# Optimization experiments

Hardware: AMD Instinct MI355X
Metric: run time of the kernel (lower is better)

Reference implementation:

```python
import jax, jax.numpy as jnp
import numpy as np

N = 50000
E = 800000
IN_C, HID, OUT_C = 128, 128, 40
EPS = 1e-5  # BatchNorm eps


def setup_inputs() -> dict:
    key = jax.random.key(0)
    ks = jax.random.split(key, 8)
    x = jax.random.normal(ks[0], (N, IN_C), dtype=jnp.float32)
    edge_index = jax.random.randint(ks[1], (2, E), 0, N, dtype=jnp.int64)
    s1 = 1.0 / np.sqrt(IN_C)
    s2 = 1.0 / np.sqrt(HID)
    return {
        "x": x,
        "edge_index": edge_index,
        "W1": jax.random.uniform(ks[2], (IN_C, HID), jnp.float32, -s1, s1),
        "b1": jnp.zeros((HID,), jnp.float32),
        "g1": jnp.ones((HID,), jnp.float32),
        "beta1": jnp.zeros((HID,), jnp.float32),
        "W2": jax.random.uniform(ks[3], (HID, HID), jnp.float32, -s2, s2),
        "b2": jnp.zeros((HID,), jnp.float32),
        "g2": jnp.ones((HID,), jnp.float32),
        "beta2": jnp.zeros((HID,), jnp.float32),
        "W3": jax.random.uniform(ks[4], (HID, OUT_C), jnp.float32, -s2, s2),
        "b3": jnp.zeros((OUT_C,), jnp.float32),
    }


def _gcn_norm(src, dst, num_nodes):
    # symmetric normalization D^-1/2 A D^-1/2, no self loops, unit edge weights
    deg = jax.ops.segment_sum(jnp.ones_like(dst, dtype=jnp.float32), dst,
                              num_segments=num_nodes)
    dinv = jnp.where(deg > 0, jax.lax.rsqrt(jnp.maximum(deg, 1.0)), 0.0)
    return dinv[src] * dinv[dst]  # [E]


def _conv(h, W, b, src, dst, norm, num_nodes):
    h = h @ W  # linear transform first (fewer message features)
    msg = norm[:, None] * h[src]  # [E, F] gather
    out = jax.ops.segment_sum(msg, dst, num_segments=num_nodes)  # scatter-add
    return out + b


def _bn_relu(h, g, beta):
    mu = jnp.mean(h, axis=0)
    var = jnp.mean(jnp.square(h - mu), axis=0)  # biased, as torch BN
    hn = (h - mu) * jax.lax.rsqrt(var + EPS) * g + beta
    return jax.nn.relu(hn)


def reference(x, edge_index, W1, b1, g1, beta1, W2, b2, g2, beta2, W3, b3):
    src, dst = edge_index[0], edge_index[1]
    norm = _gcn_norm(src, dst, N)  # cached=True: shared across layers
    h = _bn_relu(_conv(x, W1, b1, src, dst, norm, N), g1, beta1)
    h = _bn_relu(_conv(h, W2, b2, src, dst, norm, N), g2, beta2)
    return _conv(h, W3, b3, src, dst, norm, N)
```

## Files before the change

kernel.cpp:

```cpp
#include <hip/hip_runtime.h>
#include <hip/hip_fp16.h>

typedef _Float16 half8 __attribute__((ext_vector_type(8)));
typedef float floatx4 __attribute__((ext_vector_type(4)));


__device__ __forceinline__ void unpack8(uint4 v, float* f) {
    const __half2* hp = (const __half2*)&v;
    float2 a = __half22float2(hp[0]);
    float2 b = __half22float2(hp[1]);
    float2 c = __half22float2(hp[2]);
    float2 d = __half22float2(hp[3]);
    f[0] = a.x; f[1] = a.y; f[2] = b.x; f[3] = b.y;
    f[4] = c.x; f[5] = c.y; f[6] = d.x; f[7] = d.y;
}

__device__ __forceinline__ uint4 pack8(const float* f) {
    __half2 h0 = __floats2half2_rn(f[0], f[1]);
    __half2 h1 = __floats2half2_rn(f[2], f[3]);
    __half2 h2 = __floats2half2_rn(f[4], f[5]);
    __half2 h3 = __floats2half2_rn(f[6], f[7]);
    uint4 v;
    v.x = *(const unsigned int*)&h0;
    v.y = *(const unsigned int*)&h1;
    v.z = *(const unsigned int*)&h2;
    v.w = *(const unsigned int*)&h3;
    return v;
}

__global__ void k_zeroz(int* p, int n) {
    int i = blockIdx.x * 256 + threadIdx.x;
    if (i < n) p[i] = 0;
}


__global__ void k_packW3(const float* __restrict__ W1, const float* __restrict__ W2,
                         const float* __restrict__ W3, __half* __restrict__ Wt1,
                         __half* __restrict__ Wt2, __half* __restrict__ Wt3) {
    int i = blockIdx.x * 256 + threadIdx.x;
    if (i < 128 * 128) {
        int n = i >> 7, k = i & 127;
        Wt1[i] = __float2half(W1[(size_t)k * 128 + n]);
    } else if (i < 2 * 128 * 128) {
        int j = i - 128 * 128;
        int n = j >> 7, k = j & 127;
        Wt2[j] = __float2half(W2[(size_t)k * 128 + n]);
    } else if (i < 2 * 128 * 128 + 48 * 128) {
        int j = i - 2 * 128 * 128;
        int n = j >> 7, k = j & 127;
        Wt3[j] = (n < 40) ? __float2half(W3[(size_t)k * 40 + n]) : __half(0.f);
    }
}


__global__ void k_deg_xcd(const int* __restrict__ dst, int* __restrict__ deg,
                          int E, int rs) {
    int lo = (blockIdx.x & 7) * rs;
    int i = (blockIdx.x >> 3) * 256 + threadIdx.x;
    if (i < E) {
        int d = dst[i];
        if (d >= lo && d < lo + rs) atomicAdd(&deg[d], 1);
    }
}

__global__ void k_place_xcd(const int* __restrict__ src, const int* __restrict__ dst,
                            int* __restrict__ cursor, unsigned short* __restrict__ sidx,
                            int E, int rs) {
    int lo = (blockIdx.x & 7) * rs;
    int i = (blockIdx.x >> 3) * 256 + threadIdx.x;
    if (i < E) {
        int d = dst[i];
        if (d >= lo && d < lo + rs) {
            int pos = atomicAdd(&cursor[d], 1);
            sidx[pos] = (unsigned short)src[i];
        }
    }
}

__global__ __launch_bounds__(256) void k_chunkscan(const int* __restrict__ deg,
                                                   int* __restrict__ bsum, int n) {
    __shared__ int ls[256];
    int t = threadIdx.x;
    int s = 0;
    int base = t * 256;
    for (int k = 0; k < 256; ++k) {
        int idx = base + k;
        if (idx < n) s += deg[idx];
    }
    ls[t] = s;
    __syncthreads();
    for (int off = 1; off < 256; off <<= 1) {
        int v = t >= off ? ls[t - off] : 0;
        __syncthreads();
        ls[t] += v;
        __syncthreads();
    }
    bsum[t] = ls[t] - s;
}

__global__ void k_scanchunk(const int* __restrict__ cnt, const int* __restrict__ bsum,
                            int* __restrict__ row_ptr, int* __restrict__ cursor,
                            float* __restrict__ dinv, int n, int E) {
    __shared__ int ls[256];
    int i = blockIdx.x * 256 + threadIdx.x;
    int v = i < n ? cnt[i] : 0;
    ls[threadIdx.x] = v;
    __syncthreads();
    for (int off = 1; off < 256; off <<= 1) {
        int t = threadIdx.x >= off ? ls[threadIdx.x - off] : 0;
        __syncthreads();
        ls[threadIdx.x] += t;
        __syncthreads();
    }
    if (i < n) {
        int ex = ls[threadIdx.x] - v + bsum[blockIdx.x];
        row_ptr[i] = ex;
        cursor[i] = ex;
        dinv[i] = v > 0 ? rsqrtf((float)v) : 0.f;
    }
    if (i == n - 1) row_ptr[n] = E;
}


template <int CT, int STRIDE, int VALID, int AMODE, int CSPLIT>
__global__ __launch_bounds__(256) void k_gemm_mfma(const void* __restrict__ Ap,
                                                   const __half* __restrict__ Wt,
                                                   const float* __restrict__ sums32,
                                                   const float* __restrict__ sumsq32,
                                                   const float* __restrict__ g,
                                                   const float* __restrict__ beta,
                                                   const float* __restrict__ dinv,
                                                   __half* __restrict__ C, int nrows) {
    __shared__ char lw[CT * 16 * 256];
    __shared__ float lsc[128], lsh[128];
    const int rowblk = (CSPLIT == 2) ? (blockIdx.x >> 1) : blockIdx.x;
    const int colblk = (CSPLIT == 2) ? (blockIdx.x & 1) : 0;

    const int nu4 = CT * 16 * 16;
    for (int i = threadIdx.x; i < nu4; i += 256) {
        int row = i >> 4, k8 = i & 15;
        uint4 v = ((const uint4*)Wt)[(colblk * CT * 16 + row) * 16 + k8];
        *(uint4*)(lw + ((row * 256 + k8 * 16) ^ ((row & 7) << 4))) = v;
    }
    if (AMODE == 1 && threadIdx.x < 128) {
        int c = threadIdx.x;
        float s = 0.f, q = 0.f;
        for (int k2 = 0; k2 < 32; ++k2) {
            s += sums32[k2 * 128 + c];
            q += sumsq32[k2 * 128 + c];
        }
        float inv_n = 1.f / (float)nrows;
        float mu = s * inv_n;
        float var = q * inv_n - mu * mu;
        float rs = rsqrtf(var + 1e-5f);
        float sc = rs * g[c];
        lsc[c] = sc;
        lsh[c] = beta[c] - mu * sc;
    }
    __syncthreads();

    const int lane = threadIdx.x & 63;
    const int wid = threadIdx.x >> 6;
    const int l15 = lane & 15;
    const int lg = lane >> 4;
    const int rowbase = rowblk * 128 + wid * 32;

    half8 a2[2][4];
#pragma unroll
    for (int r = 0; r < 2; ++r) {
        int row = rowbase + r * 16 + l15;
        bool ok = row < nrows;
#pragma unroll
        for (int kk = 0; kk < 4; ++kk) {
            const int c0 = kk * 32 + lg * 8;
            half8 h = {0, 0, 0, 0, 0, 0, 0, 0};
            if (ok) {
                if (AMODE == 0) {
                    const float* a = (const float*)Ap + (size_t)row * 128 + c0;
                    float4 v0 = *(const float4*)a;
                    float4 v1 = *(const float4*)(a + 4);
                    h[0] = (_Float16)v0.x; h[1] = (_Float16)v0.y;
                    h[2] = (_Float16)v0.z; h[3] = (_Float16)v0.w;
                    h[4] = (_Float16)v1.x; h[5] = (_Float16)v1.y;
                    h[6] = (_Float16)v1.z; h[7] = (_Float16)v1.w;
                } else {
                    uint4 raw = *(const uint4*)((const __half*)Ap + (size_t)row * 128 + c0);
                    float f[8];
                    unpack8(raw, f);
                    float4 s0 = *(const float4*)&lsc[c0];
                    float4 s1 = *(const float4*)&lsc[c0 + 4];
                    float4 t0 = *(const float4*)&lsh[c0];
                    float4 t1 = *(const float4*)&lsh[c0 + 4];
                    h[0] = (_Float16)fmaxf(f[0] * s0.x + t0.x, 0.f);
                    h[1] = (_Float16)fmaxf(f[1] * s0.y + t0.y, 0.f);
                    h[2] = (_Float16)fmaxf(f[2] * s0.z + t0.z, 0.f);
                    h[3] = (_Float16)fmaxf(f[3] * s0.w + t0.w, 0.f);
                    h[4] = (_Float16)fmaxf(f[4] * s1.x + t1.x, 0.f);
                    h[5] = (_Float16)fmaxf(f[5] * s1.y + t1.y, 0.f);
                    h[6] = (_Float16)fmaxf(f[6] * s1.z + t1.z, 0.f);
                    h[7] = (_Float16)fmaxf(f[7] * s1.w + t1.w, 0.f);
                }
            }
            a2[r][kk] = h;
        }
    }

    floatx4 acc[2][CT];
#pragma unroll
    for (int r = 0; r < 2; ++r)
#pragma unroll
        for (int c = 0; c < CT; ++c) acc[r][c] = (floatx4){0.f, 0.f, 0.f, 0.f};

#pragma unroll
    for (int kk = 0; kk < 4; ++kk) {
#pragma unroll
        for (int c = 0; c < CT; ++c) {
            int wrow = c * 16 + l15;
            half8 bfrag = *(const half8*)(lw + ((wrow * 256 + kk * 64 + lg * 16) ^ ((wrow & 7) << 4)));
#pragma unroll
            for (int r = 0; r < 2; ++r)
                acc[r][c] = __builtin_amdgcn_mfma_f32_16x16x32_f16(a2[r][kk], bfrag, acc[r][c], 0, 0, 0);
        }
    }

    if (CSPLIT == 2) {
        __syncthreads();
        __half* ct = (__half*)lw;
#pragma unroll
        for (int r = 0; r < 2; ++r) {
            int lr0 = wid * 32 + r * 16 + lg * 4;
            float d4[4];
#pragma unroll
            for (int j = 0; j < 4; ++j) {
                int row = rowblk * 128 + lr0 + j;
                d4[j] = row < nrows ? dinv[row] : 0.f;
            }
#pragma unroll
            for (int c = 0; c < CT; ++c) {
                int col = c * 16 + l15;
#pragma unroll
                for (int j = 0; j < 4; ++j) {
                    int lrow = lr0 + j;
                    int cc = col ^ (((lrow >> 2) & 1) << 5);
                    ct[lrow * 64 + cc] = __float2half(acc[r][c][j] * d4[j]);
                }
            }
        }
        __syncthreads();
        for (int i = threadIdx.x; i < 128 * 8; i += 256) {
            int lrow = i >> 3, u = i & 7;
            int row = rowblk * 128 + lrow;
            if (row < nrows) {
                int cc = (u * 8) ^ (((lrow >> 2) & 1) << 5);
                uint4 v = *(const uint4*)&ct[lrow * 64 + cc];
                *(uint4*)(&C[(size_t)row * STRIDE + colblk * 64 + u * 8]) = v;
            }
        }
    } else {
#pragma unroll
        for (int r = 0; r < 2; ++r) {
            int rbase = rowbase + r * 16 + lg * 4;
            float d4[4];
#pragma unroll
            for (int j = 0; j < 4; ++j)
                d4[j] = (rbase + j) < nrows ? dinv[rbase + j] : 0.f;
#pragma unroll
            for (int c = 0; c < CT; ++c) {
                int col = c * 16 + l15;
                if (VALID != CT * 16 && col >= VALID) continue;
#pragma unroll
                for (int j = 0; j < 4; ++j) {
                    int row = rbase + j;
                    if (row < nrows)
                        C[(size_t)row * STRIDE + col] = __float2half(acc[r][c][j] * d4[j]);
                }
            }
        }
    }
}


__global__ __launch_bounds__(256) void k_agg128_stats(const __half* __restrict__ M,
                                                      const int* __restrict__ rp,
                                                      const unsigned short* __restrict__ sidx,
                                                      const float* __restrict__ dinv,
                                                      __half* __restrict__ Hout,
                                                      float* __restrict__ sums32,
                                                      float* __restrict__ sumsq32, int n) {
    int d = blockIdx.x * 16 + (threadIdx.x >> 4);
    int lane = threadIdx.x & 15;
    float acc[8] = {0.f, 0.f, 0.f, 0.f, 0.f, 0.f, 0.f, 0.f};
    if (d < n) {
        int beg = rp[d], end = rp[d + 1];
        int j = beg;
        for (; j + 4 <= end; j += 4) {
            int s0 = sidx[j], s1 = sidx[j + 1], s2 = sidx[j + 2], s3 = sidx[j + 3];
            uint4 v0 = *(const uint4*)(M + (size_t)s0 * 128 + lane * 8);
            uint4 v1 = *(const uint4*)(M + (size_t)s1 * 128 + lane * 8);
            uint4 v2 = *(const uint4*)(M + (size_t)s2 * 128 + lane * 8);
            uint4 v3 = *(const uint4*)(M + (size_t)s3 * 128 + lane * 8);
            float f0[8], f1[8], f2[8], f3[8];
            unpack8(v0, f0); unpack8(v1, f1); unpack8(v2, f2); unpack8(v3, f3);
#pragma unroll
            for (int i = 0; i < 8; ++i)
                acc[i] += (f0[i] + f1[i]) + (f2[i] + f3[i]);
        }
        for (; j < end; ++j) {
            int s = sidx[j];
            uint4 v = *(const uint4*)(M + (size_t)s * 128 + lane * 8);
            float f[8];
            unpack8(v, f);
#pragma unroll
            for (int i = 0; i < 8; ++i) acc[i] += f[i];
        }
        float sc = dinv[d];
#pragma unroll
        for (int i = 0; i < 8; ++i) acc[i] *= sc;
        *(uint4*)(Hout + (size_t)d * 128 + lane * 8) = pack8(acc);
    }
    float sq[8];
#pragma unroll
    for (int i = 0; i < 8; ++i) sq[i] = acc[i] * acc[i];
#pragma unroll
    for (int m = 16; m <= 32; m <<= 1) {
#pragma unroll
        for (int i = 0; i < 8; ++i) {
            acc[i] += __shfl_xor(acc[i], m);
            sq[i]  += __shfl_xor(sq[i], m);
        }
    }
    __shared__ float lsw[2][4][16][8];
    int wid = threadIdx.x >> 6, wl = threadIdx.x & 63;
    if (wl < 16) {
#pragma unroll
        for (int i = 0; i < 8; ++i) {
            lsw[0][wid][wl][i] = acc[i];
            lsw[1][wid][wl][i] = sq[i];
        }
    }
    __syncthreads();
    if (threadIdx.x < 128) {
        int c = threadIdx.x;
        int lc = c >> 3, e = c & 7;
        float ss = 0.f, qq = 0.f;
#pragma unroll
        for (int w = 0; w < 4; ++w) {
            ss += lsw[0][w][lc][e];
            qq += lsw[1][w][lc][e];
        }
        int sh = (blockIdx.x & 31) * 128;
        atomicAdd(&sums32[sh + c], ss);
        atomicAdd(&sumsq32[sh + c], qq);
    }
}


__global__ void k_agg40_f16(const __half* __restrict__ M,
                            const int* __restrict__ rp,
                            const unsigned short* __restrict__ sidx,
                            const float* __restrict__ dinv,
                            const float* __restrict__ b3,
                            float* __restrict__ out, int n) {
    int i = blockIdx.x * 256 + threadIdx.x;
    if (i >= n * 5) return;
    int d = i / 5, q = i % 5;
    int beg = rp[d], end = rp[d + 1];
    float acc[8] = {0.f, 0.f, 0.f, 0.f, 0.f, 0.f, 0.f, 0.f};
    int j = beg;
    for (; j + 4 <= end; j += 4) {
        int s0 = sidx[j], s1 = sidx[j + 1], s2 = sidx[j + 2], s3 = sidx[j + 3];
        uint4 v0 = *(const uint4*)(M + (size_t)s0 * 64 + q * 8);
        uint4 v1 = *(const uint4*)(M + (size_t)s1 * 64 + q * 8);
        uint4 v2 = *(const uint4*)(M + (size_t)s2 * 64 + q * 8);
        uint4 v3 = *(const uint4*)(M + (size_t)s3 * 64 + q * 8);
        float f0[8], f1[8], f2[8], f3[8];
        unpack8(v0, f0); unpack8(v1, f1); unpack8(v2, f2); unpack8(v3, f3);
#pragma unroll
        for (int k = 0; k < 8; ++k)
            acc[k] += (f0[k] + f1[k]) + (f2[k] + f3[k]);
    }
    for (; j < end; ++j) {
        int s = sidx[j];
        uint4 v = *(const uint4*)(M + (size_t)s * 64 + q * 8);
        float f[8];
        unpack8(v, f);
#pragma unroll
        for (int k = 0; k < 8; ++k) acc[k] += f[k];
    }
    float sc = dinv[d];
    float4 b0 = *(const float4*)&b3[q * 8];
    float4 b1 = *(const float4*)&b3[q * 8 + 4];
    float4 r0, r1;
    r0.x = acc[0] * sc + b0.x; r0.y = acc[1] * sc + b0.y;
    r0.z = acc[2] * sc + b0.z; r0.w = acc[3] * sc + b0.w;
    r1.x = acc[4] * sc + b1.x; r1.y = acc[5] * sc + b1.y;
    r1.z = acc[6] * sc + b1.z; r1.w = acc[7] * sc + b1.w;
    float* o = out + (size_t)d * 40 + q * 8;
    *(float4*)o = r0;
    *(float4*)(o + 4) = r1;
}


extern "C" void kernel_launch(void* const* d_in, const int* in_sizes, int n_in,
                              void* d_out, int out_size, void* d_ws, size_t ws_size,
                              hipStream_t stream) {
    const float* x  = (const float*)d_in[0];
    const int*   ei = (const int*)d_in[1];
    const float* W1 = (const float*)d_in[2];
    const float* g1 = (const float*)d_in[4];
    const float* be1= (const float*)d_in[5];
    const float* W2 = (const float*)d_in[6];
    const float* g2 = (const float*)d_in[8];
    const float* be2= (const float*)d_in[9];
    const float* W3 = (const float*)d_in[10];
    const float* b3 = (const float*)d_in[11];

    const int N = in_sizes[0] / 128;
    const int E = in_sizes[1] / 2;
    const int* srcv = ei;
    const int* dstv = ei + E;
    const int NB = (N + 255) / 256;
    const int RS = (N + 7) / 8;
    const int EB8 = 8 * ((E + 255) / 256);

    __half* M    = (__half*)d_ws;
    __half* Hb   = M + (size_t)N * 128;
    __half* t3   = Hb + (size_t)N * 128;
    __half* Wt1  = t3 + (size_t)N * 64;
    __half* Wt2  = Wt1 + 128 * 128;
    __half* Wt3  = Wt2 + 128 * 128;
    float* dinv    = (float*)(Wt3 + 48 * 128);
    int*   deg     = (int*)(dinv + N);
    float* sumsA   = (float*)(deg + N);
    float* sumsqA  = sumsA + 32 * 128;
    float* sumsB   = sumsqA + 32 * 128;
    float* sumsqB  = sumsB + 32 * 128;
    int*   row_ptr = (int*)(sumsqB + 32 * 128);
    int*   cursor  = row_ptr + N + 1;
    unsigned short* sidx = (unsigned short*)(cursor + N);
    int*   bsum    = (int*)(sidx + E);
    float* out     = (float*)d_out;

    const int GB = (N + 127) / 128;
    const int ZN = N + 4 * 32 * 128;

    k_packW3<<<(2 * 128 * 128 + 48 * 128 + 255) / 256, 256, 0, stream>>>(W1, W2, W3, Wt1, Wt2, Wt3);
    k_zeroz<<<(ZN + 255) / 256, 256, 0, stream>>>(deg, ZN);
    k_deg_xcd<<<EB8, 256, 0, stream>>>(dstv, deg, E, RS);
    k_chunkscan<<<1, 256, 0, stream>>>(deg, bsum, N);
    k_scanchunk<<<NB, 256, 0, stream>>>(deg, bsum, row_ptr, cursor, dinv, N, E);
    k_place_xcd<<<EB8, 256, 0, stream>>>(srcv, dstv, cursor, sidx, E, RS);

    k_gemm_mfma<4, 128, 128, 0, 2><<<GB * 2, 256, 0, stream>>>(x, Wt1, nullptr, nullptr, nullptr, nullptr, dinv, M, N);
    k_agg128_stats<<<(N + 15) / 16, 256, 0, stream>>>(M, row_ptr, sidx, dinv, Hb, sumsA, sumsqA, N);

    k_gemm_mfma<4, 128, 128, 1, 2><<<GB * 2, 256, 0, stream>>>(Hb, Wt2, sumsA, sumsqA, g1, be1, dinv, M, N);
    k_agg128_stats<<<(N + 15) / 16, 256, 0, stream>>>(M, row_ptr, sidx, dinv, Hb, sumsB, sumsqB, N);

    k_gemm_mfma<3, 64, 40, 1, 1><<<GB, 256, 0, stream>>>(Hb, Wt3, sumsB, sumsqB, g2, be2, dinv, t3, N);
    k_agg40_f16<<<(N * 5 + 255) / 256, 256, 0, stream>>>(t3, row_ptr, sidx, dinv, b3, out, N);
}
```

Measured before the change: 228.2 us.

## Fuse setup kernels, prefetch GEMM inputs early, stage all GEMM stores, deepen gather unroll

Merges weight packing and buffer zeroing into one setup kernel, which removes a launch. The GEMM now issues its activation loads before the weight staging and barrier so their latency overlaps the LDS fill. The layer-3 GEMM output now goes through LDS for coalesced 16-byte stores instead of scalar half stores. The 128-wide aggregation gets an 8-edge unrolled loop for more loads in flight. In exchange, register pressure rises in both the GEMM and the gather loop.

```diff
diff --git a/kernel.cpp b/kernel.cpp
--- a/kernel.cpp
+++ b/kernel.cpp
@@ -28,15 +28,12 @@
     return v;
 }
 
-__global__ void k_zeroz(int* p, int n) {
-    int i = blockIdx.x * 256 + threadIdx.x;
-    if (i < n) p[i] = 0;
-}
-
-
-__global__ void k_packW3(const float* __restrict__ W1, const float* __restrict__ W2,
-                         const float* __restrict__ W3, __half* __restrict__ Wt1,
-                         __half* __restrict__ Wt2, __half* __restrict__ Wt3) {
+
+__global__ void k_setup(const float* __restrict__ W1, const float* __restrict__ W2,
+                        const float* __restrict__ W3, __half* __restrict__ Wt1,
+                        __half* __restrict__ Wt2, __half* __restrict__ Wt3,
+                        int* __restrict__ zp, int zn) {
+    const int PW = 2 * 128 * 128 + 48 * 128;
     int i = blockIdx.x * 256 + threadIdx.x;
     if (i < 128 * 128) {
         int n = i >> 7, k = i & 127;
@@ -45,10 +42,13 @@
         int j = i - 128 * 128;
         int n = j >> 7, k = j & 127;
         Wt2[j] = __float2half(W2[(size_t)k * 128 + n]);
-    } else if (i < 2 * 128 * 128 + 48 * 128) {
+    } else if (i < PW) {
         int j = i - 2 * 128 * 128;
         int n = j >> 7, k = j & 127;
         Wt3[j] = (n < 40) ? __float2half(W3[(size_t)k * 40 + n]) : __half(0.f);
+    } else {
+        int j = i - PW;
+        if (j < zn) zp[j] = 0;
     }
 }
 
@@ -131,15 +131,42 @@
                                                    const float* __restrict__ beta,
                                                    const float* __restrict__ dinv,
                                                    __half* __restrict__ C, int nrows) {
+    constexpr int CW = CT * 16;
     __shared__ char lw[CT * 16 * 256];
     __shared__ float lsc[128], lsh[128];
     const int rowblk = (CSPLIT == 2) ? (blockIdx.x >> 1) : blockIdx.x;
     const int colblk = (CSPLIT == 2) ? (blockIdx.x & 1) : 0;
 
+    const int lane = threadIdx.x & 63;
+    const int wid = threadIdx.x >> 6;
+    const int l15 = lane & 15;
+    const int lg = lane >> 4;
+    const int rowbase = rowblk * 128 + wid * 32;
+
+    uint4 raw16[2][4];
+    float4 raw32[2][4][2];
+#pragma unroll
+    for (int r = 0; r < 2; ++r) {
+        int row = rowbase + r * 16 + l15;
+        bool ok = row < nrows;
+#pragma unroll
+        for (int kk = 0; kk < 4; ++kk) {
+            const int c0 = kk * 32 + lg * 8;
+            if (AMODE == 0) {
+                const float* a = (const float*)Ap + (size_t)row * 128 + c0;
+                raw32[r][kk][0] = ok ? *(const float4*)a : make_float4(0.f, 0.f, 0.f, 0.f);
+                raw32[r][kk][1] = ok ? *(const float4*)(a + 4) : make_float4(0.f, 0.f, 0.f, 0.f);
+            } else {
+                raw16[r][kk] = ok ? *(const uint4*)((const __half*)Ap + (size_t)row * 128 + c0)
+                                  : make_uint4(0, 0, 0, 0);
+            }
+        }
+    }
+
     const int nu4 = CT * 16 * 16;
     for (int i = threadIdx.x; i < nu4; i += 256) {
         int row = i >> 4, k8 = i & 15;
-        uint4 v = ((const uint4*)Wt)[(colblk * CT * 16 + row) * 16 + k8];
+        uint4 v = ((const uint4*)Wt)[(colblk * CW + row) * 16 + k8];
         *(uint4*)(lw + ((row * 256 + k8 * 16) ^ ((row & 7) << 4))) = v;
     }
     if (AMODE == 1 && threadIdx.x < 128) {
@@ -159,47 +186,35 @@
     }
     __syncthreads();
 
-    const int lane = threadIdx.x & 63;
-    const int wid = threadIdx.x >> 6;
-    const int l15 = lane & 15;
-    const int lg = lane >> 4;
-    const int rowbase = rowblk * 128 + wid * 32;
-
     half8 a2[2][4];
 #pragma unroll
     for (int r = 0; r < 2; ++r) {
-        int row = rowbase + r * 16 + l15;
-        bool ok = row < nrows;
 #pragma unroll
         for (int kk = 0; kk < 4; ++kk) {
             const int c0 = kk * 32 + lg * 8;
-            half8 h = {0, 0, 0, 0, 0, 0, 0, 0};
-            if (ok) {
-                if (AMODE == 0) {
-                    const float* a = (const float*)Ap + (size_t)row * 128 + c0;
-                    float4 v0 = *(const float4*)a;
-                    float4 v1 = *(const float4*)(a + 4);
-                    h[0] = (_Float16)v0.x; h[1] = (_Float16)v0.y;
-                    h[2] = (_Float16)v0.z; h[3] = (_Float16)v0.w;
-                    h[4] = (_Float16)v1.x; h[5] = (_Float16)v1.y;
-                    h[6] = (_Float16)v1.z; h[7] = (_Float16)v1.w;
-                } else {
-                    uint4 raw = *(const uint4*)((const __half*)Ap + (size_t)row * 128 + c0);
-                    float f[8];
-                    unpack8(raw, f);
-                    float4 s0 = *(const float4*)&lsc[c0];
-                    float4 s1 = *(const float4*)&lsc[c0 + 4];
-                    float4 t0 = *(const float4*)&lsh[c0];
-                    float4 t1 = *(const float4*)&lsh[c0 + 4];
-                    h[0] = (_Float16)fmaxf(f[0] * s0.x + t0.x, 0.f);
-                    h[1] = (_Float16)fmaxf(f[1] * s0.y + t0.y, 0.f);
-                    h[2] = (_Float16)fmaxf(f[2] * s0.z + t0.z, 0.f);
-                    h[3] = (_Float16)fmaxf(f[3] * s0.w + t0.w, 0.f);
-                    h[4] = (_Float16)fmaxf(f[4] * s1.x + t1.x, 0.f);
-                    h[5] = (_Float16)fmaxf(f[5] * s1.y + t1.y, 0.f);
-                    h[6] = (_Float16)fmaxf(f[6] * s1.z + t1.z, 0.f);
-                    h[7] = (_Float16)fmaxf(f[7] * s1.w + t1.w, 0.f);
-                }
+            half8 h;
+            if (AMODE == 0) {
+                float4 v0 = raw32[r][kk][0];
+                float4 v1 = raw32[r][kk][1];
+                h[0] = (_Float16)v0.x; h[1] = (_Float16)v0.y;
+                h[2] = (_Float16)v0.z; h[3] = (_Float16)v0.w;
+                h[4] = (_Float16)v1.x; h[5] = (_Float16)v1.y;
+                h[6] = (_Float16)v1.z; h[7] = (_Float16)v1.w;
+            } else {
+                float f[8];
+                unpack8(raw16[r][kk], f);
+                float4 s0 = *(const float4*)&lsc[c0];
+                float4 s1 = *(const float4*)&lsc[c0 + 4];
+                float4 t0 = *(const float4*)&lsh[c0];
+                float4 t1 = *(const float4*)&lsh[c0 + 4];
+                h[0] = (_Float16)fmaxf(f[0] * s0.x + t0.x, 0.f);
+                h[1] = (_Float16)fmaxf(f[1] * s0.y + t0.y, 0.f);
+                h[2] = (_Float16)fmaxf(f[2] * s0.z + t0.z, 0.f);
+                h[3] = (_Float16)fmaxf(f[3] * s0.w + t0.w, 0.f);
+                h[4] = (_Float16)fmaxf(f[4] * s1.x + t1.x, 0.f);
+                h[5] = (_Float16)fmaxf(f[5] * s1.y + t1.y, 0.f);
+                h[6] = (_Float16)fmaxf(f[6] * s1.z + t1.z, 0.f);
+                h[7] = (_Float16)fmaxf(f[7] * s1.w + t1.w, 0.f);
             }
             a2[r][kk] = h;
         }
@@ -223,58 +238,39 @@
         }
     }
 
-    if (CSPLIT == 2) {
-        __syncthreads();
-        __half* ct = (__half*)lw;
-#pragma unroll
-        for (int r = 0; r < 2; ++r) {
-            int lr0 = wid * 32 + r * 16 + lg * 4;
-            float d4[4];
+    const int BV = (VALID - colblk * CW) < CW ? (VALID - colblk * CW) : CW;
+    __syncthreads();
+    __half* ct = (__half*)lw;
+#pragma unroll
+    for (int r = 0; r < 2; ++r) {
+        int lr0 = wid * 32 + r * 16 + lg * 4;
+        float d4[4];
+#pragma unroll
+        for (int j = 0; j < 4; ++j) {
+            int row = rowblk * 128 + lr0 + j;
+            d4[j] = row < nrows ? dinv[row] : 0.f;
+        }
+#pragma unroll
+        for (int c = 0; c < CT; ++c) {
+            int col = c * 16 + l15;
 #pragma unroll
             for (int j = 0; j < 4; ++j) {
-                int row = rowblk * 128 + lr0 + j;
-                d4[j] = row < nrows ? dinv[row] : 0.f;
+                int lrow = lr0 + j;
+                int cc = (CW == 64) ? (col ^ (((lrow >> 2) & 1) << 5)) : col;
+                ct[lrow * CW + cc] = __float2half(acc[r][c][j] * d4[j]);
             }
-#pragma unroll
-            for (int c = 0; c < CT; ++c) {
-                int col = c * 16 + l15;
-#pragma unroll
-                for (int j = 0; j < 4; ++j) {
-                    int lrow = lr0 + j;
-                    int cc = col ^ (((lrow >> 2) & 1) << 5);
-                    ct[lrow * 64 + cc] = __float2half(acc[r][c][j] * d4[j]);
-                }
-            }
-        }
-        __syncthreads();
-        for (int i = threadIdx.x; i < 128 * 8; i += 256) {
-            int lrow = i >> 3, u = i & 7;
-            int row = rowblk * 128 + lrow;
-            if (row < nrows) {
-                int cc = (u * 8) ^ (((lrow >> 2) & 1) << 5);
-                uint4 v = *(const uint4*)&ct[lrow * 64 + cc];
-                *(uint4*)(&C[(size_t)row * STRIDE + colblk * 64 + u * 8]) = v;
-            }
-        }
-    } else {
-#pragma unroll
-        for (int r = 0; r < 2; ++r) {
-            int rbase = rowbase + r * 16 + lg * 4;
-            float d4[4];
-#pragma unroll
-            for (int j = 0; j < 4; ++j)
-                d4[j] = (rbase + j) < nrows ? dinv[rbase + j] : 0.f;
-#pragma unroll
-            for (int c = 0; c < CT; ++c) {
-                int col = c * 16 + l15;
-                if (VALID != CT * 16 && col >= VALID) continue;
-#pragma unroll
-                for (int j = 0; j < 4; ++j) {
-                    int row = rbase + j;
-                    if (row < nrows)
-                        C[(size_t)row * STRIDE + col] = __float2half(acc[r][c][j] * d4[j]);
-                }
-            }
+        }
+    }
+    __syncthreads();
+    constexpr int U = CW / 8;
+    for (int i = threadIdx.x; i < 128 * U; i += 256) {
+        int lrow = i / U, u = i % U;
+        int row = rowblk * 128 + lrow;
+        int col0 = u * 8;
+        if (row < nrows && col0 < BV) {
+            int cc = (CW == 64) ? (col0 ^ (((lrow >> 2) & 1) << 5)) : col0;
+            uint4 v = *(const uint4*)&ct[lrow * CW + cc];
+            *(uint4*)(&C[(size_t)row * STRIDE + colblk * CW + col0]) = v;
         }
     }
 }
@@ -293,21 +289,34 @@
     if (d < n) {
         int beg = rp[d], end = rp[d + 1];
         int j = beg;
+        for (; j + 8 <= end; j += 8) {
+            uint4 v[8];
+#pragma unroll
+            for (int t = 0; t < 8; ++t)
+                v[t] = *(const uint4*)(M + (size_t)sidx[j + t] * 128 + lane * 8);
+#pragma unroll
+            for (int t = 0; t < 8; ++t) {
+                float f[8];
+                unpack8(v[t], f);
+#pragma unroll
+                for (int i = 0; i < 8; ++i) acc[i] += f[i];
+            }
+        }
         for (; j + 4 <= end; j += 4) {
-            int s0 = sidx[j], s1 = sidx[j + 1], s2 = sidx[j + 2], s3 = sidx[j + 3];
-            uint4 v0 = *(const uint4*)(M + (size_t)s0 * 128 + lane * 8);
-            uint4 v1 = *(const uint4*)(M + (size_t)s1 * 128 + lane * 8);
-            uint4 v2 = *(const uint4*)(M + (size_t)s2 * 128 + lane * 8);
-            uint4 v3 = *(const uint4*)(M + (size_t)s3 * 128 + lane * 8);
-            float f0[8], f1[8], f2[8], f3[8];
-            unpack8(v0, f0); unpack8(v1, f1); unpack8(v2, f2); unpack8(v3, f3);
-#pragma unroll
-            for (int i = 0; i < 8; ++i)
-                acc[i] += (f0[i] + f1[i]) + (f2[i] + f3[i]);
+            uint4 v[4];
+#pragma unroll
+            for (int t = 0; t < 4; ++t)
+                v[t] = *(const uint4*)(M + (size_t)sidx[j + t] * 128 + lane * 8);
+#pragma unroll
+            for (int t = 0; t < 4; ++t) {
+                float f[8];
+                unpack8(v[t], f);
+#pragma unroll
+                for (int i = 0; i < 8; ++i) acc[i] += f[i];
+            }
         }
         for (; j < end; ++j) {
-            int s = sidx[j];
-            uint4 v = *(const uint4*)(M + (size_t)s * 128 + lane * 8);
+            uint4 v = *(const uint4*)(M + (size_t)sidx[j] * 128 + lane * 8);
             float f[8];
             unpack8(v, f);
 #pragma unroll
@@ -368,11 +377,10 @@
     float acc[8] = {0.f, 0.f, 0.f, 0.f, 0.f, 0.f, 0.f, 0.f};
     int j = beg;
     for (; j + 4 <= end; j += 4) {
-        int s0 = sidx[j], s1 = sidx[j + 1], s2 = sidx[j + 2], s3 = sidx[j + 3];
-        uint4 v0 = *(const uint4*)(M + (size_t)s0 * 64 + q * 8);
-        uint4 v1 = *(const uint4*)(M + (size_t)s1 * 64 + q * 8);
-        uint4 v2 = *(const uint4*)(M + (size_t)s2 * 64 + q * 8);
-        uint4 v3 = *(const uint4*)(M + (size_t)s3 * 64 + q * 8);
+        uint4 v0 = *(const uint4*)(M + (size_t)sidx[j] * 64 + q * 8);
+        uint4 v1 = *(const uint4*)(M + (size_t)sidx[j + 1] * 64 + q * 8);
+        uint4 v2 = *(const uint4*)(M + (size_t)sidx[j + 2] * 64 + q * 8);
+        uint4 v3 = *(const uint4*)(M + (size_t)sidx[j + 3] * 64 + q * 8);
         float f0[8], f1[8], f2[8], f3[8];
         unpack8(v0, f0); unpack8(v1, f1); unpack8(v2, f2); unpack8(v3, f3);
 #pragma unroll
@@ -380,8 +388,7 @@
             acc[k] += (f0[k] + f1[k]) + (f2[k] + f3[k]);
     }
     for (; j < end; ++j) {
-        int s = sidx[j];
-        uint4 v = *(const uint4*)(M + (size_t)s * 64 + q * 8);
+        uint4 v = *(const uint4*)(M + (size_t)sidx[j] * 64 + q * 8);
         float f[8];
         unpack8(v, f);
 #pragma unroll
@@ -443,9 +450,9 @@
 
     const int GB = (N + 127) / 128;
     const int ZN = N + 4 * 32 * 128;
-
-    k_packW3<<<(2 * 128 * 128 + 48 * 128 + 255) / 256, 256, 0, stream>>>(W1, W2, W3, Wt1, Wt2, Wt3);
-    k_zeroz<<<(ZN + 255) / 256, 256, 0, stream>>>(deg, ZN);
+    const int SETUP_TOT = 2 * 128 * 128 + 48 * 128 + ZN;
+
+    k_setup<<<(SETUP_TOT + 255) / 256, 256, 0, stream>>>(W1, W2, W3, Wt1, Wt2, Wt3, deg, ZN);
     k_deg_xcd<<<EB8, 256, 0, stream>>>(dstv, deg, E, RS);
     k_chunkscan<<<1, 256, 0, stream>>>(deg, bsum, N);
     k_scanchunk<<<NB, 256, 0, stream>>>(deg, bsum, row_ptr, cursor, dinv, N, E);
```

After: 229.1 us. No clear change (+0.4%).
